# Kernel tuning notes

Measured on AMD Instinct MI355X. Metric: run time of the kernel, lower is better.

## Reference

```python
import math
import jax, jax.numpy as jnp
import numpy as np

B, L, NS = 8, 1024, 512
D, NH, DN = 512, 8, 256
E, K, HE = 8, 2, 2048
EPS = 1e-5


def setup_inputs() -> dict:
    key = jax.random.key(0)
    ks = jax.random.split(key, 40)
    def rn(i, shape, s=0.02):
        return jax.random.normal(ks[i], shape, jnp.float32) * s
    inp = {
        'x': jax.random.normal(ks[0], (B, L, D), jnp.float32),
        'scene_tokens': jax.random.normal(ks[1], (B, NS, D), jnp.float32),
        't': jax.random.uniform(ks[2], (B,), jnp.float32) * 1000.0,
        # scene LayerNorm (affine)
        'scene_norm_g': jnp.ones((D,), jnp.float32),
        'scene_norm_b': jnp.zeros((D,), jnp.float32),
        # scene cross-attn projections (stored [in,out])
        'ca_wq': rn(3, (D, D)), 'ca_bq': jnp.zeros((D,)),
        'ca_wk': rn(4, (D, D)), 'ca_bk': jnp.zeros((D,)),
        'ca_wv': rn(5, (D, D)), 'ca_bv': jnp.zeros((D,)),
        'ca_wo': rn(6, (D, D)), 'ca_bo': jnp.zeros((D,)),
        # self-attn projections
        'sa_wq': rn(7, (D, D)), 'sa_bq': jnp.zeros((D,)),
        'sa_wk': rn(8, (D, D)), 'sa_bk': jnp.zeros((D,)),
        'sa_wv': rn(9, (D, D)), 'sa_bv': jnp.zeros((D,)),
        'sa_wo': rn(10, (D, D)), 'sa_bo': jnp.zeros((D,)),
        # noise_embed MLP: Linear(D,DN) -> SiLU -> Linear(DN,DN)
        'ne_w1': rn(11, (D, DN)), 'ne_b1': jnp.zeros((DN,)),
        'ne_w2': rn(12, (DN, DN)), 'ne_b2': jnp.zeros((DN,)),
        # AdaLN modulations: Linear(DN, 2D)
        'ncsa_mod_w': rn(13, (DN, 2 * D)), 'ncsa_mod_b': jnp.zeros((2 * D,)),
        'moe_mod_w': rn(14, (DN, 2 * D)), 'moe_mod_b': jnp.zeros((2 * D,)),
        # router
        'router_w': rn(15, (DN, E), s=0.1),
        # stacked pose-branch experts: fc_in D->2*HE, fc_out HE->D
        'fc_in_w': rn(16, (E, D, 2 * HE)), 'fc_in_b': jnp.zeros((E, 2 * HE)),
        'fc_out_w': rn(17, (E, HE, D)), 'fc_out_b': jnp.zeros((E, D)),
    }
    return inp


def _ln(x):
    mu = x.mean(-1, keepdims=True)
    var = ((x - mu) ** 2).mean(-1, keepdims=True)
    return (x - mu) * jax.lax.rsqrt(var + EPS)


def _mha(q_in, k_in, v_in, wq, bq, wk, bk, wv, bv, wo, bo):
    b, lq, d = q_in.shape
    lk = k_in.shape[1]
    hd = d // NH
    q = (q_in @ wq + bq).reshape(b, lq, NH, hd)
    k = (k_in @ wk + bk).reshape(b, lk, NH, hd)
    v = (v_in @ wv + bv).reshape(b, lk, NH, hd)
    att = jnp.einsum('bqhd,bkhd->bhqk', q, k) / math.sqrt(hd)
    p = jax.nn.softmax(att, axis=-1)
    o = jnp.einsum('bhqk,bkhd->bqhd', p, v).reshape(b, lq, d)
    return o @ wo + bo


def reference(x, scene_tokens, t,
              scene_norm_g, scene_norm_b,
              ca_wq, ca_bq, ca_wk, ca_bk, ca_wv, ca_bv, ca_wo, ca_bo,
              sa_wq, sa_bq, sa_wk, sa_bk, sa_wv, sa_bv, sa_wo, sa_bo,
              ne_w1, ne_b1, ne_w2, ne_b2,
              ncsa_mod_w, ncsa_mod_b, moe_mod_w, moe_mod_b,
              router_w, fc_in_w, fc_in_b, fc_out_w, fc_out_b):
    # --- noise clock embedding: sinusoidal(t, D) -> MLP ---
    half = D // 2
    freqs = jnp.exp(-math.log(10000.0) * jnp.arange(half, dtype=jnp.float32) / (half - 1))
    ang = t[:, None] * freqs[None, :]
    temb = jnp.concatenate([jnp.cos(ang), jnp.sin(ang)], axis=-1)  # [B, D]
    nc = jax.nn.silu(temb @ ne_w1 + ne_b1) @ ne_w2 + ne_b2  # [B, DN]

    # --- scene cross-attention ---
    x_in = _ln(x) * scene_norm_g + scene_norm_b
    x = x + _mha(x_in, scene_tokens, scene_tokens,
                 ca_wq, ca_bq, ca_wk, ca_bk, ca_wv, ca_bv, ca_wo, ca_bo)

    # --- noise-conditioned self-attention (AdaLN) ---
    mod = nc @ ncsa_mod_w + ncsa_mod_b
    shift, scale = jnp.split(mod, 2, axis=-1)
    x_ncsa = _ln(x) * (1.0 + scale[:, None, :]) + shift[:, None, :]
    x = x + _mha(x_ncsa, x_ncsa, x_ncsa,
                 sa_wq, sa_bq, sa_wk, sa_bk, sa_wv, sa_bv, sa_wo, sa_bo)

    # --- pose branch: AdaLN + noise-conditioned MoE ---
    mod = nc @ moe_mod_w + moe_mod_b
    shift, scale = jnp.split(mod, 2, axis=-1)
    x_moe = _ln(x) * (1.0 + scale[:, None, :]) + shift[:, None, :]

    logits = nc @ router_w  # temperature = 1.0
    probs = jax.nn.softmax(logits, axis=-1)
    tw, ti = jax.lax.top_k(probs, K)  # [B,K]
    tw = tw / jnp.clip(tw.sum(-1, keepdims=True), 1e-8)

    # gather per-sample selected expert weights -> grouped GEMM
    Wi = fc_in_w[ti]   # [B,K,D,2HE]
    bi = fc_in_b[ti]   # [B,K,2HE]
    h = jnp.einsum('bld,bkdh->bklh', x_moe, Wi) + bi[:, :, None, :]
    val, gate = jnp.split(h, 2, axis=-1)
    hid = val * jax.nn.silu(gate)   # [B,K,L,HE]
    Wo = fc_out_w[ti]  # [B,K,HE,D]
    bo = fc_out_b[ti]  # [B,K,D]
    eo = jnp.einsum('bklh,bkhd->bkld', hid, Wo) + bo[:, :, None, :]
    mixed = jnp.einsum('bk,bkld->bld', tw, eo)

    return x + mixed
```

## Files before the change

kernel.cpp:

```cpp
#include <hip/hip_runtime.h>
#include <math.h>

typedef unsigned short ushort_t;
typedef __attribute__((ext_vector_type(8))) short short8;
typedef __attribute__((ext_vector_type(4))) float f32x4;

#define B_   8
#define L_   1024
#define NS_  512
#define D_   512
#define NH_  8
#define HE_  2048
#define EPS_ 1e-5f

#define MFMA16(a, b, c) __builtin_amdgcn_mfma_f32_16x16x32_bf16(a, b, c, 0, 0, 0)
#define GL2LDS(g, l) __builtin_amdgcn_global_load_lds( \
    (const __attribute__((address_space(1))) unsigned int*)(g), \
    (__attribute__((address_space(3))) unsigned int*)(l), 16, 0, 0)

__device__ __forceinline__ ushort_t f2bf(float f) {
  unsigned u = __float_as_uint(f);
  unsigned r = (u + 0x7fffu + ((u >> 16) & 1u)) >> 16;
  return (ushort_t)r;
}

__device__ __forceinline__ void stage_tile(const ushort_t* __restrict__ g0,
                                           int ld, ushort_t* lds) {
  const int t = threadIdx.x;
  const int w = t >> 6, lane = t & 63;
#pragma unroll
  for (int j = 0; j < 2; ++j) {
    const int c = w * 64 + j * 256 + lane;
    const int row = c >> 2, col = (c & 3) * 8;
    GL2LDS(g0 + (size_t)row * ld + col, lds + (size_t)(w * 64 + j * 256) * 8);
  }
}

__global__ __launch_bounds__(256) void noise_embed(
    const float* __restrict__ t_in,
    const float* __restrict__ w1, const float* __restrict__ b1,
    const float* __restrict__ w2, const float* __restrict__ b2,
    const float* __restrict__ rw,
    float* __restrict__ nc_out,
    float* __restrict__ tw_out, int* __restrict__ ti_out)
{
  const int b = blockIdx.x;
  const int t = threadIdx.x;
  __shared__ float temb[512];
  __shared__ float h1[256];
  __shared__ float ncs[256];
  const float tv = t_in[b];
  {
    float fr = __expf(-logf(10000.0f) * (float)t / 255.0f);
    float ang = tv * fr;
    temb[t] = cosf(ang);
    temb[256 + t] = sinf(ang);
  }
  __syncthreads();
  {
    float s = b1[t];
#pragma unroll 8
    for (int i = 0; i < 512; ++i) s += temb[i] * w1[i * 256 + t];
    h1[t] = s / (1.0f + __expf(-s));
  }
  __syncthreads();
  {
    float s = b2[t];
#pragma unroll 8
    for (int i = 0; i < 256; ++i) s += h1[i] * w2[i * 256 + t];
    ncs[t] = s;
    nc_out[b * 256 + t] = s;
  }
  __syncthreads();
  if (t == 0) {
    float lg[8];
    for (int e = 0; e < 8; ++e) {
      float s = 0.f;
      for (int i = 0; i < 256; ++i) s += ncs[i] * rw[i * 8 + e];
      lg[e] = s;
    }
    float mx = lg[0];
    for (int e = 1; e < 8; ++e) mx = fmaxf(mx, lg[e]);
    float z = 0.f, p[8];
    for (int e = 0; e < 8; ++e) { p[e] = __expf(lg[e] - mx); z += p[e]; }
    for (int e = 0; e < 8; ++e) p[e] /= z;
    int i0 = 0;
    for (int e = 1; e < 8; ++e) if (p[e] > p[i0]) i0 = e;
    int i1 = (i0 == 0) ? 1 : 0;
    for (int e = 0; e < 8; ++e) if (e != i0 && p[e] > p[i1]) i1 = e;
    float s01 = fmaxf(p[i0] + p[i1], 1e-8f);
    tw_out[b * 2 + 0] = p[i0] / s01;
    tw_out[b * 2 + 1] = p[i1] / s01;
    ti_out[b * 2 + 0] = i0;
    ti_out[b * 2 + 1] = i1;
  }
}

__global__ __launch_bounds__(256) void mod_proj(
    const float* __restrict__ nc,
    const float* __restrict__ ncsa_w, const float* __restrict__ ncsa_b,
    const float* __restrict__ moe_w, const float* __restrict__ moe_b,
    float* __restrict__ ncsa_mod, float* __restrict__ moe_mod)
{
  const int b = blockIdx.x, cg = blockIdx.y;
  const int t = threadIdx.x;
  __shared__ float ncs[256];
  ncs[t] = nc[b * 256 + t];
  __syncthreads();
  const int col = cg * 128 + (t & 127);
  const int half = t >> 7;
  const float* wsel = half ? moe_w : ncsa_w;
  const float* bsel = half ? moe_b : ncsa_b;
  float* osel = half ? moe_mod : ncsa_mod;
  float s = bsel[col];
#pragma unroll 8
  for (int i = 0; i < 256; ++i) s += ncs[i] * wsel[(size_t)i * 1024 + col];
  osel[b * 1024 + col] = s;
}

__global__ __launch_bounds__(256) void ln_mod_kernel(
    const float* __restrict__ X, const float* __restrict__ gvec,
    const float* __restrict__ bvec, const float* __restrict__ mod,
    ushort_t* __restrict__ Y)
{
  const int row = blockIdx.x;
  const int b = row >> 10;
  const int t = threadIdx.x;
  const float* xr = X + (size_t)row * 512;
  float2 v = *(const float2*)(xr + t * 2);
  float s = v.x + v.y;
  float q = v.x * v.x + v.y * v.y;
#pragma unroll
  for (int off = 32; off > 0; off >>= 1) {
    s += __shfl_down(s, off, 64);
    q += __shfl_down(q, off, 64);
  }
  __shared__ float ws_[4], wq_[4], smu[1], sinv[1];
  if ((t & 63) == 0) { ws_[t >> 6] = s; wq_[t >> 6] = q; }
  __syncthreads();
  if (t == 0) {
    float S = ws_[0] + ws_[1] + ws_[2] + ws_[3];
    float Q = wq_[0] + wq_[1] + wq_[2] + wq_[3];
    float mu = S * (1.0f / 512.0f);
    float var = Q * (1.0f / 512.0f) - mu * mu;
    smu[0] = mu;
    sinv[0] = rsqrtf(var + EPS_);
  }
  __syncthreads();
  const float mu = smu[0], inv = sinv[0];
  const int d0 = t * 2;
  float scx, scy, shx, shy;
  if (mod) {
    const float* mrow = mod + (size_t)b * 1024;
    scx = 1.0f + mrow[512 + d0]; scy = 1.0f + mrow[512 + d0 + 1];
    shx = mrow[d0];              shy = mrow[d0 + 1];
  } else {
    scx = gvec[d0]; scy = gvec[d0 + 1];
    shx = bvec[d0]; shy = bvec[d0 + 1];
  }
  float ox = (v.x - mu) * inv * scx + shx;
  float oy = (v.y - mu) * inv * scy + shy;
  unsigned pk = (unsigned)f2bf(ox) | ((unsigned)f2bf(oy) << 16);
  *(unsigned*)(Y + (size_t)row * 512 + d0) = pk;
}

__global__ __launch_bounds__(256) void transpose_cvt(
    const float* __restrict__ in, ushort_t* __restrict__ out,
    int R, int C, long ibs, long obs)
{
  __shared__ float tile[32][33];
  const float* src = in + (size_t)blockIdx.z * ibs;
  ushort_t* dst = out + (size_t)blockIdx.z * obs;
  const int c0 = blockIdx.x * 32, r0 = blockIdx.y * 32;
  const int tx = threadIdx.x & 31, ty = threadIdx.x >> 5;
  for (int rr = ty; rr < 32; rr += 8)
    tile[rr][tx] = src[(size_t)(r0 + rr) * C + c0 + tx];
  __syncthreads();
  for (int rr = ty; rr < 32; rr += 8)
    dst[(size_t)(c0 + rr) * R + r0 + tx] = f2bf(tile[tx][rr]);
}

struct P8 { const float* p[8]; };
__global__ __launch_bounds__(256) void transpose_cvt8(
    P8 srcs, ushort_t* __restrict__ out)
{
  __shared__ float tile[32][33];
  const float* src = srcs.p[blockIdx.z];
  ushort_t* dst = out + (size_t)blockIdx.z * 512 * 512;
  const int c0 = blockIdx.x * 32, r0 = blockIdx.y * 32;
  const int tx = threadIdx.x & 31, ty = threadIdx.x >> 5;
  for (int rr = ty; rr < 32; rr += 8)
    tile[rr][tx] = src[(size_t)(r0 + rr) * 512 + c0 + tx];
  __syncthreads();
  for (int rr = ty; rr < 32; rr += 8)
    dst[(size_t)(c0 + rr) * 512 + r0 + tx] = f2bf(tile[tx][rr]);
}

__global__ __launch_bounds__(256) void cvt_bf16(
    const float* __restrict__ in, ushort_t* __restrict__ out)
{
  const int i = (blockIdx.x * 256 + threadIdx.x) * 4;
  float4 v = *(const float4*)(in + i);
  uint2 pk;
  pk.x = (unsigned)f2bf(v.x) | ((unsigned)f2bf(v.y) << 16);
  pk.y = (unsigned)f2bf(v.z) | ((unsigned)f2bf(v.w) << 16);
  *(uint2*)(out + i) = pk;
}

__global__ __launch_bounds__(256) void gemm_bf16(
    const ushort_t* __restrict__ A, const ushort_t* __restrict__ Bt,
    const float* __restrict__ bias, const float* __restrict__ resid,
    void* __restrict__ Cout, int M, int N, int K, int bf16_out)
{
  __shared__ ushort_t As[2][4096];
  __shared__ ushort_t Bs[2][4096];
  const int t = threadIdx.x;
  const int w = t >> 6, lane = t & 63;
  const int quad = lane >> 4, r = lane & 15;
  const int wm = w >> 1, wn = w & 1;
  const int bm = blockIdx.y * 128, bn = blockIdx.x * 128;
  f32x4 acc[4][4];
#pragma unroll
  for (int i = 0; i < 4; ++i)
#pragma unroll
    for (int j = 0; j < 4; ++j) acc[i][j] = (f32x4){0.f, 0.f, 0.f, 0.f};
  const ushort_t* Ab = A + (size_t)bm * K;
  const ushort_t* Bb = Bt + (size_t)bn * K;
  const int NIT = K >> 5;
  stage_tile(Ab, K, As[0]);
  stage_tile(Bb, K, Bs[0]);
  __syncthreads();
  for (int it = 0; it < NIT; ++it) {
    const int cur = it & 1;
    if (it + 1 < NIT) {
      stage_tile(Ab + (it + 1) * 32, K, As[cur ^ 1]);
      stage_tile(Bb + (it + 1) * 32, K, Bs[cur ^ 1]);
    }
    short8 af[4], bfg[4];
#pragma unroll
    for (int i = 0; i < 4; ++i)
      af[i] = *(const short8*)&As[cur][(wm * 64 + i * 16 + r) * 32 + quad * 8];
#pragma unroll
    for (int j = 0; j < 4; ++j)
      bfg[j] = *(const short8*)&Bs[cur][(wn * 64 + j * 16 + r) * 32 + quad * 8];
#pragma unroll
    for (int i = 0; i < 4; ++i)
#pragma unroll
      for (int j = 0; j < 4; ++j)
        acc[i][j] = MFMA16(af[i], bfg[j], acc[i][j]);
    __syncthreads();
  }
  if (bf16_out) {
    ushort_t* Cb = (ushort_t*)Cout;
#pragma unroll
    for (int j = 0; j < 4; ++j) {
      const int col = bn + wn * 64 + j * 16 + r;
      const float bia = bias[col];
#pragma unroll
      for (int i = 0; i < 4; ++i)
#pragma unroll
        for (int reg = 0; reg < 4; ++reg) {
          const int row = bm + wm * 64 + i * 16 + quad * 4 + reg;
          Cb[(size_t)row * N + col] = f2bf(acc[i][j][reg] + bia);
        }
    }
  } else {
    float* Cf = (float*)Cout;
#pragma unroll
    for (int j = 0; j < 4; ++j) {
      const int col = bn + wn * 64 + j * 16 + r;
      const float bia = bias[col];
#pragma unroll
      for (int i = 0; i < 4; ++i)
#pragma unroll
        for (int reg = 0; reg < 4; ++reg) {
          const int row = bm + wm * 64 + i * 16 + quad * 4 + reg;
          float v = acc[i][j][reg] + bia;
          if (resid) v += resid[(size_t)row * N + col];
          Cf[(size_t)row * N + col] = v;
        }
    }
  }
}

__global__ __launch_bounds__(256, 2) void fattn_mfma(
    const ushort_t* __restrict__ Q, const ushort_t* __restrict__ Kmat,
    const ushort_t* __restrict__ V, ushort_t* __restrict__ O, int Lk)
{
  __shared__ __align__(16) ushort_t Ks[64][72];
  __shared__ __align__(16) ushort_t Vt[64][72];
  __shared__ __align__(16) ushort_t Pt[4][32][72];
  const int t = threadIdx.x;
  const int w = t >> 6, lane = t & 63;
  const int quad = lane >> 4, r = lane & 15;
  const int h = blockIdx.y, b = blockIdx.z;
  const int q0 = blockIdx.x * 128;
  const size_t hoff = (size_t)h * 64;
  const ushort_t* Qb = Q + ((size_t)b * 1024 + q0) * 512 + hoff;
  const ushort_t* Kb = Kmat + (size_t)b * Lk * 512 + hoff;
  const ushort_t* Vb = V + (size_t)b * Lk * 512 + hoff;

  short8 qb[2][2];
#pragma unroll
  for (int ct = 0; ct < 2; ++ct)
#pragma unroll
    for (int ki = 0; ki < 2; ++ki)
      qb[ct][ki] = *(const short8*)(Qb + (size_t)(w * 32 + ct * 16 + r) * 512 +
                                    ki * 32 + quad * 8);

  f32x4 oacc[4][2];
#pragma unroll
  for (int rt = 0; rt < 4; ++rt)
#pragma unroll
    for (int ct = 0; ct < 2; ++ct) oacc[rt][ct] = (f32x4){0.f, 0.f, 0.f, 0.f};
  float m_[2] = {-1e30f, -1e30f};
  float l_[2] = {0.f, 0.f};

  uint4 kr[2], vr[2], kn[2], vn[2];
  auto ldkv = [&](int k0, uint4* kp, uint4* vp) {
#pragma unroll
    for (int j = 0; j < 2; ++j) {
      const int dof = (w + 4 * j) * 8;
      kp[j] = *(const uint4*)(Kb + (size_t)(k0 + lane) * 512 + dof);
      vp[j] = *(const uint4*)(Vb + (size_t)(k0 + lane) * 512 + dof);
    }
  };
  auto stkv = [&](const uint4* kp, const uint4* vp) {
#pragma unroll
    for (int j = 0; j < 2; ++j) {
      const int dof = (w + 4 * j) * 8;
      *(uint4*)&Ks[lane][dof] = kp[j];
      const ushort_t* vv = (const ushort_t*)&vp[j];
#pragma unroll
      for (int i = 0; i < 8; ++i) Vt[dof + i][lane] = vv[i];
    }
  };

  ldkv(0, kr, vr);
  const int nch = Lk >> 6;
  for (int c = 0; c < nch; ++c) {
    stkv(kr, vr);
    __syncthreads();
    if (c + 1 < nch) ldkv((c + 1) << 6, kn, vn);

    f32x4 sacc[4][2];
#pragma unroll
    for (int rt = 0; rt < 4; ++rt)
#pragma unroll
      for (int ct = 0; ct < 2; ++ct) sacc[rt][ct] = (f32x4){0.f, 0.f, 0.f, 0.f};
#pragma unroll
    for (int ki = 0; ki < 2; ++ki) {
      short8 kf[4];
#pragma unroll
      for (int rt = 0; rt < 4; ++rt)
        kf[rt] = *(const short8*)&Ks[rt * 16 + r][ki * 32 + quad * 8];
#pragma unroll
      for (int rt = 0; rt < 4; ++rt)
#pragma unroll
        for (int ct = 0; ct < 2; ++ct)
          sacc[rt][ct] = MFMA16(kf[rt], qb[ct][ki], sacc[rt][ct]);
    }

#pragma unroll
    for (int ct = 0; ct < 2; ++ct) {
      float vmax = sacc[0][ct][0];
#pragma unroll
      for (int rt = 0; rt < 4; ++rt)
#pragma unroll
        for (int reg = 0; reg < 4; ++reg) vmax = fmaxf(vmax, sacc[rt][ct][reg]);
      vmax = fmaxf(vmax, __shfl_xor(vmax, 16, 64));
      vmax = fmaxf(vmax, __shfl_xor(vmax, 32, 64));
      const float mnew = fmaxf(m_[ct], vmax * 0.125f);
      const float corr = __expf(m_[ct] - mnew);
      m_[ct] = mnew;
      float ps = 0.f;
#pragma unroll
      for (int rt = 0; rt < 4; ++rt) {
        float p0 = __expf(fmaf(sacc[rt][ct][0], 0.125f, -mnew));
        float p1 = __expf(fmaf(sacc[rt][ct][1], 0.125f, -mnew));
        float p2 = __expf(fmaf(sacc[rt][ct][2], 0.125f, -mnew));
        float p3 = __expf(fmaf(sacc[rt][ct][3], 0.125f, -mnew));
        ps += (p0 + p1) + (p2 + p3);
        uint2 pk;
        pk.x = (unsigned)f2bf(p0) | ((unsigned)f2bf(p1) << 16);
        pk.y = (unsigned)f2bf(p2) | ((unsigned)f2bf(p3) << 16);
        *(uint2*)&Pt[w][ct * 16 + r][rt * 16 + quad * 4] = pk;
      }
      ps += __shfl_xor(ps, 16, 64);
      ps += __shfl_xor(ps, 32, 64);
      l_[ct] = l_[ct] * corr + ps;
#pragma unroll
      for (int rt = 0; rt < 4; ++rt)
#pragma unroll
        for (int reg = 0; reg < 4; ++reg) oacc[rt][ct][reg] *= corr;
    }

#pragma unroll
    for (int ki = 0; ki < 2; ++ki) {
      short8 vf[4], pf[2];
#pragma unroll
      for (int rt = 0; rt < 4; ++rt)
        vf[rt] = *(const short8*)&Vt[rt * 16 + r][ki * 32 + quad * 8];
#pragma unroll
      for (int ct = 0; ct < 2; ++ct)
        pf[ct] = *(const short8*)&Pt[w][ct * 16 + r][ki * 32 + quad * 8];
#pragma unroll
      for (int rt = 0; rt < 4; ++rt)
#pragma unroll
        for (int ct = 0; ct < 2; ++ct)
          oacc[rt][ct] = MFMA16(vf[rt], pf[ct], oacc[rt][ct]);
    }
    __syncthreads();
#pragma unroll
    for (int j = 0; j < 2; ++j) { kr[j] = kn[j]; vr[j] = vn[j]; }
  }

#pragma unroll
  for (int ct = 0; ct < 2; ++ct) {
    const float inv = 1.0f / l_[ct];
    const int qg = q0 + w * 32 + ct * 16 + r;
    ushort_t* op = O + ((size_t)b * 1024 + qg) * 512 + hoff;
#pragma unroll
    for (int rt = 0; rt < 4; ++rt) {
      uint2 pk;
      pk.x = (unsigned)f2bf(oacc[rt][ct][0] * inv) |
             ((unsigned)f2bf(oacc[rt][ct][1] * inv) << 16);
      pk.y = (unsigned)f2bf(oacc[rt][ct][2] * inv) |
             ((unsigned)f2bf(oacc[rt][ct][3] * inv) << 16);
      *(uint2*)(op + rt * 16 + quad * 4) = pk;
    }
  }
}

__global__ __launch_bounds__(256) void moe_fcin(
    const ushort_t* __restrict__ Xm, const ushort_t* __restrict__ WiT,
    const float* __restrict__ Bi, const float* __restrict__ tw,
    const int* __restrict__ ti, ushort_t* __restrict__ Hid, int ks)
{
  __shared__ ushort_t As[2][4096];
  __shared__ ushort_t Bv[2][4096];
  __shared__ ushort_t Bg[2][4096];
  const int t = threadIdx.x;
  const int w = t >> 6, lane = t & 63;
  const int quad = lane >> 4, r = lane & 15;
  const int wm = w >> 1, wn = w & 1;
  const int b = blockIdx.z;
  const int e = ti[b * 2 + ks];
  const float wq = tw[b * 2 + ks];
  const int r0 = blockIdx.y * 128, n0 = blockIdx.x * 128;
  const ushort_t* Ab = Xm + ((size_t)b * 1024 + r0) * 512;
  const ushort_t* Wv = WiT + (size_t)e * 4096 * 512 + (size_t)n0 * 512;
  const ushort_t* Wg = Wv + (size_t)2048 * 512;
  f32x4 av[4][4], ag[4][4];
#pragma unroll
  for (int i = 0; i < 4; ++i)
#pragma unroll
    for (int j = 0; j < 4; ++j) {
      av[i][j] = (f32x4){0.f, 0.f, 0.f, 0.f};
      ag[i][j] = (f32x4){0.f, 0.f, 0.f, 0.f};
    }
  stage_tile(Ab, 512, As[0]);
  stage_tile(Wv, 512, Bv[0]);
  stage_tile(Wg, 512, Bg[0]);
  __syncthreads();
  for (int it = 0; it < 16; ++it) {
    const int cur = it & 1;
    if (it + 1 < 16) {
      stage_tile(Ab + (it + 1) * 32, 512, As[cur ^ 1]);
      stage_tile(Wv + (it + 1) * 32, 512, Bv[cur ^ 1]);
      stage_tile(Wg + (it + 1) * 32, 512, Bg[cur ^ 1]);
    }
    short8 af[4], bv[4], bg[4];
#pragma unroll
    for (int i = 0; i < 4; ++i)
      af[i] = *(const short8*)&As[cur][(wm * 64 + i * 16 + r) * 32 + quad * 8];
#pragma unroll
    for (int j = 0; j < 4; ++j) {
      bv[j] = *(const short8*)&Bv[cur][(wn * 64 + j * 16 + r) * 32 + quad * 8];
      bg[j] = *(const short8*)&Bg[cur][(wn * 64 + j * 16 + r) * 32 + quad * 8];
    }
#pragma unroll
    for (int i = 0; i < 4; ++i)
#pragma unroll
      for (int j = 0; j < 4; ++j) {
        av[i][j] = MFMA16(af[i], bv[j], av[i][j]);
        ag[i][j] = MFMA16(af[i], bg[j], ag[i][j]);
      }
    __syncthreads();
  }
  ushort_t* Hb = Hid + (size_t)b * 1024 * 2048;
#pragma unroll
  for (int j = 0; j < 4; ++j) {
    const int col = n0 + wn * 64 + j * 16 + r;
    const float bval = Bi[(size_t)e * 4096 + col];
    const float bgat = Bi[(size_t)e * 4096 + 2048 + col];
#pragma unroll
    for (int i = 0; i < 4; ++i)
#pragma unroll
      for (int reg = 0; reg < 4; ++reg) {
        const int lrow = r0 + wm * 64 + i * 16 + quad * 4 + reg;
        float vv = av[i][j][reg] + bval;
        float gg = ag[i][j][reg] + bgat;
        float hv = vv * (gg / (1.0f + __expf(-gg))) * wq;
        Hb[(size_t)lrow * 2048 + col] = f2bf(hv);
      }
  }
}

__global__ __launch_bounds__(256) void moe_fcout(
    const ushort_t* __restrict__ Hid, const ushort_t* __restrict__ WoT,
    const float* __restrict__ Bo, const float* __restrict__ X2,
    const float* __restrict__ tw, const int* __restrict__ ti,
    float* __restrict__ Out, int ks, int first)
{
  __shared__ ushort_t As[2][4096];
  __shared__ ushort_t Bs[2][4096];
  const int t = threadIdx.x;
  const int w = t >> 6, lane = t & 63;
  const int quad = lane >> 4, r = lane & 15;
  const int wm = w >> 1, wn = w & 1;
  const int b = blockIdx.z;
  const int e = ti[b * 2 + ks];
  const int r0 = blockIdx.y * 128, n0 = blockIdx.x * 128;
  f32x4 acc[4][4];
#pragma unroll
  for (int i = 0; i < 4; ++i)
#pragma unroll
    for (int j = 0; j < 4; ++j) acc[i][j] = (f32x4){0.f, 0.f, 0.f, 0.f};
  const ushort_t* Ab = Hid + ((size_t)b * 1024 + r0) * 2048;
  const ushort_t* Bb = WoT + (size_t)e * 512 * 2048 + (size_t)n0 * 2048;
  stage_tile(Ab, 2048, As[0]);
  stage_tile(Bb, 2048, Bs[0]);
  __syncthreads();
  for (int it = 0; it < 64; ++it) {
    const int cur = it & 1;
    if (it + 1 < 64) {
      stage_tile(Ab + (it + 1) * 32, 2048, As[cur ^ 1]);
      stage_tile(Bb + (it + 1) * 32, 2048, Bs[cur ^ 1]);
    }
    short8 af[4], bfg[4];
#pragma unroll
    for (int i = 0; i < 4; ++i)
      af[i] = *(const short8*)&As[cur][(wm * 64 + i * 16 + r) * 32 + quad * 8];
#pragma unroll
    for (int j = 0; j < 4; ++j)
      bfg[j] = *(const short8*)&Bs[cur][(wn * 64 + j * 16 + r) * 32 + quad * 8];
#pragma unroll
    for (int i = 0; i < 4; ++i)
#pragma unroll
      for (int j = 0; j < 4; ++j)
        acc[i][j] = MFMA16(af[i], bfg[j], acc[i][j]);
    __syncthreads();
  }
  const int e0 = ti[b * 2], e1 = ti[b * 2 + 1];
  const float tw0 = tw[b * 2], tw1 = tw[b * 2 + 1];
#pragma unroll
  for (int j = 0; j < 4; ++j) {
    const int col = n0 + wn * 64 + j * 16 + r;
    const float badd = first ? (tw0 * Bo[(size_t)e0 * 512 + col] +
                                tw1 * Bo[(size_t)e1 * 512 + col]) : 0.f;
#pragma unroll
    for (int i = 0; i < 4; ++i)
#pragma unroll
      for (int reg = 0; reg < 4; ++reg) {
        const size_t row = (size_t)b * 1024 + r0 + wm * 64 + i * 16 + quad * 4 + reg;
        const size_t idx = row * 512 + col;
        const float base = first ? X2[idx] : Out[idx];
        Out[idx] = base + acc[i][j][reg] + badd;
      }
  }
}

extern "C" void kernel_launch(void* const* d_in, const int* in_sizes, int n_in,
                              void* d_out, int out_size, void* d_ws, size_t ws_size,
                              hipStream_t stream) {
  const float* x        = (const float*)d_in[0];
  const float* scene    = (const float*)d_in[1];
  const float* t_in     = (const float*)d_in[2];
  const float* sn_g     = (const float*)d_in[3];
  const float* sn_b     = (const float*)d_in[4];
  const float* ca_wq    = (const float*)d_in[5];
  const float* ca_bq    = (const float*)d_in[6];
  const float* ca_wk    = (const float*)d_in[7];
  const float* ca_bk    = (const float*)d_in[8];
  const float* ca_wv    = (const float*)d_in[9];
  const float* ca_bv    = (const float*)d_in[10];
  const float* ca_wo    = (const float*)d_in[11];
  const float* ca_bo    = (const float*)d_in[12];
  const float* sa_wq    = (const float*)d_in[13];
  const float* sa_bq    = (const float*)d_in[14];
  const float* sa_wk    = (const float*)d_in[15];
  const float* sa_bk    = (const float*)d_in[16];
  const float* sa_wv    = (const float*)d_in[17];
  const float* sa_bv    = (const float*)d_in[18];
  const float* sa_wo    = (const float*)d_in[19];
  const float* sa_bo    = (const float*)d_in[20];
  const float* ne_w1    = (const float*)d_in[21];
  const float* ne_b1    = (const float*)d_in[22];
  const float* ne_w2    = (const float*)d_in[23];
  const float* ne_b2    = (const float*)d_in[24];
  const float* ncsa_w   = (const float*)d_in[25];
  const float* ncsa_b   = (const float*)d_in[26];
  const float* moe_w    = (const float*)d_in[27];
  const float* moe_b    = (const float*)d_in[28];
  const float* router_w = (const float*)d_in[29];
  const float* fc_in_w  = (const float*)d_in[30];
  const float* fc_in_b  = (const float*)d_in[31];
  const float* fc_out_w = (const float*)d_in[32];
  const float* fc_out_b = (const float*)d_in[33];
  float* out = (float*)d_out;

  char* W = (char*)d_ws;
  const size_t MB = 1u << 20;
  float* ncsa_mod = (float*)W;
  float* moe_mod  = ncsa_mod + 8192;
  float* tw       = moe_mod + 8192;
  int*   ti       = (int*)(tw + 16);
  float* nc_ws    = (float*)(ti + 16);
  ushort_t* wT      = (ushort_t*)(W + 1 * MB);
  ushort_t* fciT    = (ushort_t*)(W + 5 * MB);
  ushort_t* fcoT    = (ushort_t*)(W + 37 * MB);
  ushort_t* xin_bf  = (ushort_t*)(W + 53 * MB);
  ushort_t* attn_bf = xin_bf;
  ushort_t* scene_bf= (ushort_t*)(W + 61 * MB);
  ushort_t* qf = (ushort_t*)(W + 65 * MB);
  ushort_t* kf = (ushort_t*)(W + 73 * MB);
  ushort_t* vf = (ushort_t*)(W + 81 * MB);
  ushort_t* hid = (ushort_t*)(W + 61 * MB);
  float* x1 = out;

  const int WSZ = 512 * 512;

  noise_embed<<<dim3(B_), dim3(256), 0, stream>>>(
      t_in, ne_w1, ne_b1, ne_w2, ne_b2, router_w, nc_ws, tw, ti);
  mod_proj<<<dim3(B_, 8), dim3(256), 0, stream>>>(
      nc_ws, ncsa_w, ncsa_b, moe_w, moe_b, ncsa_mod, moe_mod);

  P8 dsrc;
  dsrc.p[0] = ca_wq; dsrc.p[1] = ca_wk; dsrc.p[2] = ca_wv; dsrc.p[3] = ca_wo;
  dsrc.p[4] = sa_wq; dsrc.p[5] = sa_wk; dsrc.p[6] = sa_wv; dsrc.p[7] = sa_wo;
  transpose_cvt8<<<dim3(16, 16, 8), 256, 0, stream>>>(dsrc, wT);
  transpose_cvt<<<dim3(128, 16, 8), 256, 0, stream>>>(fc_in_w, fciT, 512, 4096,
                                                      (long)512 * 4096, (long)512 * 4096);
  transpose_cvt<<<dim3(16, 64, 8), 256, 0, stream>>>(fc_out_w, fcoT, 2048, 512,
                                                     (long)2048 * 512, (long)2048 * 512);
  cvt_bf16<<<dim3(2048), 256, 0, stream>>>(scene, scene_bf);

  ln_mod_kernel<<<dim3(8192), 256, 0, stream>>>(x, sn_g, sn_b, nullptr, xin_bf);
  gemm_bf16<<<dim3(4, 64), 256, 0, stream>>>(xin_bf, wT + 0 * WSZ, ca_bq, nullptr, qf, 8192, 512, 512, 1);
  gemm_bf16<<<dim3(4, 32), 256, 0, stream>>>(scene_bf, wT + 1 * WSZ, ca_bk, nullptr, kf, 4096, 512, 512, 1);
  gemm_bf16<<<dim3(4, 32), 256, 0, stream>>>(scene_bf, wT + 2 * WSZ, ca_bv, nullptr, vf, 4096, 512, 512, 1);
  fattn_mfma<<<dim3(8, NH_, B_), 256, 0, stream>>>(qf, kf, vf, attn_bf, NS_);
  gemm_bf16<<<dim3(4, 64), 256, 0, stream>>>(attn_bf, wT + 3 * WSZ, ca_bo, x, x1, 8192, 512, 512, 0);

  ln_mod_kernel<<<dim3(8192), 256, 0, stream>>>(x1, nullptr, nullptr, ncsa_mod, xin_bf);
  gemm_bf16<<<dim3(4, 64), 256, 0, stream>>>(xin_bf, wT + 4 * WSZ, sa_bq, nullptr, qf, 8192, 512, 512, 1);
  gemm_bf16<<<dim3(4, 64), 256, 0, stream>>>(xin_bf, wT + 5 * WSZ, sa_bk, nullptr, kf, 8192, 512, 512, 1);
  gemm_bf16<<<dim3(4, 64), 256, 0, stream>>>(xin_bf, wT + 6 * WSZ, sa_bv, nullptr, vf, 8192, 512, 512, 1);
  fattn_mfma<<<dim3(8, NH_, B_), 256, 0, stream>>>(qf, kf, vf, attn_bf, L_);
  gemm_bf16<<<dim3(4, 64), 256, 0, stream>>>(attn_bf, wT + 7 * WSZ, sa_bo, out, out, 8192, 512, 512, 0);

  ln_mod_kernel<<<dim3(8192), 256, 0, stream>>>(out, nullptr, nullptr, moe_mod, xin_bf);
  moe_fcin<<<dim3(16, 8, B_), 256, 0, stream>>>(xin_bf, fciT, fc_in_b, tw, ti, hid, 0);
  moe_fcout<<<dim3(4, 8, B_), 256, 0, stream>>>(hid, fcoT, fc_out_b, out, tw, ti, out, 0, 1);
  moe_fcin<<<dim3(16, 8, B_), 256, 0, stream>>>(xin_bf, fciT, fc_in_b, tw, ti, hid, 1);
  moe_fcout<<<dim3(4, 8, B_), 256, 0, stream>>>(hid, fcoT, fc_out_b, out, tw, ti, out, 1, 0);
}
```

Before: 832.8 us.

## Fuse QKV projections, remap attention blocks by XCD, lazy softmax rescale

Merges the separate Q/K/V (and cross-attn K/V) projection GEMMs into single wider GEMMs by relying on the transposed weights being contiguous, with a per-512-column bias pointer table, and gives the attention kernel strided Q/K/V access. The attention grid becomes 1D with an XCD-aware mapping so blocks for the same batch/head share cache, adds s_setprio around MFMA phases, and skips the online-softmax rescale unless the running max grows by more than a threshold. noise_embed and mod_proj use 1024 threads with split-K reductions over shuffles. This cuts launch count and per-kernel overhead, at the cost of more complex indexing and a threshold-based rescale that changes numerics slightly.

```diff
diff --git a/kernel.cpp b/kernel.cpp
--- a/kernel.cpp
+++ b/kernel.cpp
@@ -36,7 +36,7 @@
   }
 }
 
-__global__ __launch_bounds__(256) void noise_embed(
+__global__ __launch_bounds__(1024) void noise_embed(
     const float* __restrict__ t_in,
     const float* __restrict__ w1, const float* __restrict__ b1,
     const float* __restrict__ w2, const float* __restrict__ b2,
@@ -49,36 +49,57 @@
   __shared__ float temb[512];
   __shared__ float h1[256];
   __shared__ float ncs[256];
+  __shared__ float lg[8];
   const float tv = t_in[b];
+  if (t < 512) {
+    const int k = t & 255;
+    float fr = __expf(-logf(10000.0f) * (float)k / 255.0f);
+    float ang = tv * fr;
+    temb[t] = (t < 256) ? cosf(ang) : sinf(ang);
+  }
+  __syncthreads();
+  const int col = t >> 2, part = t & 3;
   {
-    float fr = __expf(-logf(10000.0f) * (float)t / 255.0f);
-    float ang = tv * fr;
-    temb[t] = cosf(ang);
-    temb[256 + t] = sinf(ang);
+    float s = 0.f;
+    const float* wp = w1 + (size_t)(part * 128) * 256 + col;
+    const float* tp = temb + part * 128;
+#pragma unroll 32
+    for (int i = 0; i < 128; ++i) s += tp[i] * wp[(size_t)i * 256];
+    s += __shfl_xor(s, 1, 64);
+    s += __shfl_xor(s, 2, 64);
+    if (part == 0) {
+      s += b1[col];
+      h1[col] = s / (1.0f + __expf(-s));
+    }
   }
   __syncthreads();
   {
-    float s = b1[t];
-#pragma unroll 8
-    for (int i = 0; i < 512; ++i) s += temb[i] * w1[i * 256 + t];
-    h1[t] = s / (1.0f + __expf(-s));
-  }
-  __syncthreads();
-  {
-    float s = b2[t];
-#pragma unroll 8
-    for (int i = 0; i < 256; ++i) s += h1[i] * w2[i * 256 + t];
-    ncs[t] = s;
-    nc_out[b * 256 + t] = s;
+    float s = 0.f;
+    const float* wp = w2 + (size_t)(part * 64) * 256 + col;
+    const float* hp = h1 + part * 64;
+#pragma unroll 32
+    for (int i = 0; i < 64; ++i) s += hp[i] * wp[(size_t)i * 256];
+    s += __shfl_xor(s, 1, 64);
+    s += __shfl_xor(s, 2, 64);
+    if (part == 0) {
+      s += b2[col];
+      ncs[col] = s;
+      nc_out[b * 256 + col] = s;
+    }
+  }
+  __syncthreads();
+  if (t < 64) {
+    const int e = t >> 3, seg = t & 7;
+    float s = 0.f;
+#pragma unroll
+    for (int i = 0; i < 32; ++i) s += ncs[seg * 32 + i] * rw[(seg * 32 + i) * 8 + e];
+    s += __shfl_xor(s, 1, 64);
+    s += __shfl_xor(s, 2, 64);
+    s += __shfl_xor(s, 4, 64);
+    if (seg == 0) lg[e] = s;
   }
   __syncthreads();
   if (t == 0) {
-    float lg[8];
-    for (int e = 0; e < 8; ++e) {
-      float s = 0.f;
-      for (int i = 0; i < 256; ++i) s += ncs[i] * rw[i * 8 + e];
-      lg[e] = s;
-    }
     float mx = lg[0];
     for (int e = 1; e < 8; ++e) mx = fmaxf(mx, lg[e]);
     float z = 0.f, p[8];
@@ -96,7 +117,7 @@
   }
 }
 
-__global__ __launch_bounds__(256) void mod_proj(
+__global__ __launch_bounds__(1024) void mod_proj(
     const float* __restrict__ nc,
     const float* __restrict__ ncsa_w, const float* __restrict__ ncsa_b,
     const float* __restrict__ moe_w, const float* __restrict__ moe_b,
@@ -105,17 +126,24 @@
   const int b = blockIdx.x, cg = blockIdx.y;
   const int t = threadIdx.x;
   __shared__ float ncs[256];
-  ncs[t] = nc[b * 256 + t];
-  __syncthreads();
-  const int col = cg * 128 + (t & 127);
-  const int half = t >> 7;
+  if (t < 256) ncs[t] = nc[b * 256 + t];
+  __syncthreads();
+  const int idx = t >> 2, part = t & 3;
+  const int half = idx >> 7;
+  const int col = cg * 128 + (idx & 127);
   const float* wsel = half ? moe_w : ncsa_w;
-  const float* bsel = half ? moe_b : ncsa_b;
-  float* osel = half ? moe_mod : ncsa_mod;
-  float s = bsel[col];
-#pragma unroll 8
-  for (int i = 0; i < 256; ++i) s += ncs[i] * wsel[(size_t)i * 1024 + col];
-  osel[b * 1024 + col] = s;
+  float s = 0.f;
+  const float* wp = wsel + (size_t)(part * 64) * 1024 + col;
+  const float* np = ncs + part * 64;
+#pragma unroll 32
+  for (int i = 0; i < 64; ++i) s += np[i] * wp[(size_t)i * 1024];
+  s += __shfl_xor(s, 1, 64);
+  s += __shfl_xor(s, 2, 64);
+  if (part == 0) {
+    const float* bsel = half ? moe_b : ncsa_b;
+    float* osel = half ? moe_mod : ncsa_mod;
+    osel[b * 1024 + col] = s + bsel[col];
+  }
 }
 
 __global__ __launch_bounds__(256) void ln_mod_kernel(
@@ -207,9 +235,10 @@
   *(uint2*)(out + i) = pk;
 }
 
+struct B3 { const float* p[3]; };
 __global__ __launch_bounds__(256) void gemm_bf16(
     const ushort_t* __restrict__ A, const ushort_t* __restrict__ Bt,
-    const float* __restrict__ bias, const float* __restrict__ resid,
+    B3 bias, const float* __restrict__ resid,
     void* __restrict__ Cout, int M, int N, int K, int bf16_out)
 {
   __shared__ ushort_t As[2][4096];
@@ -255,7 +284,7 @@
 #pragma unroll
     for (int j = 0; j < 4; ++j) {
       const int col = bn + wn * 64 + j * 16 + r;
-      const float bia = bias[col];
+      const float bia = bias.p[col >> 9][col & 511];
 #pragma unroll
       for (int i = 0; i < 4; ++i)
 #pragma unroll
@@ -269,7 +298,7 @@
 #pragma unroll
     for (int j = 0; j < 4; ++j) {
       const int col = bn + wn * 64 + j * 16 + r;
-      const float bia = bias[col];
+      const float bia = bias.p[col >> 9][col & 511];
 #pragma unroll
       for (int i = 0; i < 4; ++i)
 #pragma unroll
@@ -285,7 +314,8 @@
 
 __global__ __launch_bounds__(256, 2) void fattn_mfma(
     const ushort_t* __restrict__ Q, const ushort_t* __restrict__ Kmat,
-    const ushort_t* __restrict__ V, ushort_t* __restrict__ O, int Lk)
+    const ushort_t* __restrict__ V, ushort_t* __restrict__ O, int Lk,
+    int ldq, int ldkv)
 {
   __shared__ __align__(16) ushort_t Ks[64][72];
   __shared__ __align__(16) ushort_t Vt[64][72];
@@ -293,19 +323,23 @@
   const int t = threadIdx.x;
   const int w = t >> 6, lane = t & 63;
   const int quad = lane >> 4, r = lane & 15;
-  const int h = blockIdx.y, b = blockIdx.z;
-  const int q0 = blockIdx.x * 128;
+  const int bid = blockIdx.x;
+  const int xcd = bid & 7, jj = bid >> 3;
+  const int qi = jj & 7;
+  const int g = xcd + 8 * (jj >> 3);
+  const int h = g & 7, b = g >> 3;
+  const int q0 = qi * 128;
   const size_t hoff = (size_t)h * 64;
-  const ushort_t* Qb = Q + ((size_t)b * 1024 + q0) * 512 + hoff;
-  const ushort_t* Kb = Kmat + (size_t)b * Lk * 512 + hoff;
-  const ushort_t* Vb = V + (size_t)b * Lk * 512 + hoff;
+  const ushort_t* Qb = Q + ((size_t)b * 1024 + q0) * ldq + hoff;
+  const ushort_t* Kb = Kmat + (size_t)b * Lk * ldkv + hoff;
+  const ushort_t* Vb = V + (size_t)b * Lk * ldkv + hoff;
 
   short8 qb[2][2];
 #pragma unroll
   for (int ct = 0; ct < 2; ++ct)
 #pragma unroll
     for (int ki = 0; ki < 2; ++ki)
-      qb[ct][ki] = *(const short8*)(Qb + (size_t)(w * 32 + ct * 16 + r) * 512 +
+      qb[ct][ki] = *(const short8*)(Qb + (size_t)(w * 32 + ct * 16 + r) * ldq +
                                     ki * 32 + quad * 8);
 
   f32x4 oacc[4][2];
@@ -317,12 +351,12 @@
   float l_[2] = {0.f, 0.f};
 
   uint4 kr[2], vr[2], kn[2], vn[2];
-  auto ldkv = [&](int k0, uint4* kp, uint4* vp) {
+  auto ldkvf = [&](int k0, uint4* kp, uint4* vp) {
 #pragma unroll
     for (int j = 0; j < 2; ++j) {
       const int dof = (w + 4 * j) * 8;
-      kp[j] = *(const uint4*)(Kb + (size_t)(k0 + lane) * 512 + dof);
-      vp[j] = *(const uint4*)(Vb + (size_t)(k0 + lane) * 512 + dof);
+      kp[j] = *(const uint4*)(Kb + (size_t)(k0 + lane) * ldkv + dof);
+      vp[j] = *(const uint4*)(Vb + (size_t)(k0 + lane) * ldkv + dof);
     }
   };
   auto stkv = [&](const uint4* kp, const uint4* vp) {
@@ -336,18 +370,19 @@
     }
   };
 
-  ldkv(0, kr, vr);
+  ldkvf(0, kr, vr);
   const int nch = Lk >> 6;
   for (int c = 0; c < nch; ++c) {
     stkv(kr, vr);
     __syncthreads();
-    if (c + 1 < nch) ldkv((c + 1) << 6, kn, vn);
+    if (c + 1 < nch) ldkvf((c + 1) << 6, kn, vn);
 
     f32x4 sacc[4][2];
 #pragma unroll
     for (int rt = 0; rt < 4; ++rt)
 #pragma unroll
       for (int ct = 0; ct < 2; ++ct) sacc[rt][ct] = (f32x4){0.f, 0.f, 0.f, 0.f};
+    __builtin_amdgcn_s_setprio(1);
 #pragma unroll
     for (int ki = 0; ki < 2; ++ki) {
       short8 kf[4];
@@ -360,7 +395,9 @@
         for (int ct = 0; ct < 2; ++ct)
           sacc[rt][ct] = MFMA16(kf[rt], qb[ct][ki], sacc[rt][ct]);
     }
-
+    __builtin_amdgcn_s_setprio(0);
+
+    float pm[2];
 #pragma unroll
     for (int ct = 0; ct < 2; ++ct) {
       float vmax = sacc[0][ct][0];
@@ -370,16 +407,32 @@
         for (int reg = 0; reg < 4; ++reg) vmax = fmaxf(vmax, sacc[rt][ct][reg]);
       vmax = fmaxf(vmax, __shfl_xor(vmax, 16, 64));
       vmax = fmaxf(vmax, __shfl_xor(vmax, 32, 64));
-      const float mnew = fmaxf(m_[ct], vmax * 0.125f);
-      const float corr = __expf(m_[ct] - mnew);
-      m_[ct] = mnew;
+      pm[ct] = vmax * 0.125f;
+    }
+    const bool need = (pm[0] > m_[0] + 8.f) || (pm[1] > m_[1] + 8.f);
+    if (__any(need)) {
+#pragma unroll
+      for (int ct = 0; ct < 2; ++ct) {
+        const float mnew = fmaxf(m_[ct], pm[ct]);
+        const float corr = __expf(m_[ct] - mnew);
+        m_[ct] = mnew;
+        l_[ct] *= corr;
+#pragma unroll
+        for (int rt = 0; rt < 4; ++rt)
+#pragma unroll
+          for (int reg = 0; reg < 4; ++reg) oacc[rt][ct][reg] *= corr;
+      }
+    }
+#pragma unroll
+    for (int ct = 0; ct < 2; ++ct) {
+      const float mcur = m_[ct];
       float ps = 0.f;
 #pragma unroll
       for (int rt = 0; rt < 4; ++rt) {
-        float p0 = __expf(fmaf(sacc[rt][ct][0], 0.125f, -mnew));
-        float p1 = __expf(fmaf(sacc[rt][ct][1], 0.125f, -mnew));
-        float p2 = __expf(fmaf(sacc[rt][ct][2], 0.125f, -mnew));
-        float p3 = __expf(fmaf(sacc[rt][ct][3], 0.125f, -mnew));
+        float p0 = __expf(fmaf(sacc[rt][ct][0], 0.125f, -mcur));
+        float p1 = __expf(fmaf(sacc[rt][ct][1], 0.125f, -mcur));
+        float p2 = __expf(fmaf(sacc[rt][ct][2], 0.125f, -mcur));
+        float p3 = __expf(fmaf(sacc[rt][ct][3], 0.125f, -mcur));
         ps += (p0 + p1) + (p2 + p3);
         uint2 pk;
         pk.x = (unsigned)f2bf(p0) | ((unsigned)f2bf(p1) << 16);
@@ -388,13 +441,10 @@
       }
       ps += __shfl_xor(ps, 16, 64);
       ps += __shfl_xor(ps, 32, 64);
-      l_[ct] = l_[ct] * corr + ps;
-#pragma unroll
-      for (int rt = 0; rt < 4; ++rt)
-#pragma unroll
-        for (int reg = 0; reg < 4; ++reg) oacc[rt][ct][reg] *= corr;
-    }
-
+      l_[ct] += ps;
+    }
+
+    __builtin_amdgcn_s_setprio(1);
 #pragma unroll
     for (int ki = 0; ki < 2; ++ki) {
       short8 vf[4], pf[2];
@@ -410,6 +460,7 @@
         for (int ct = 0; ct < 2; ++ct)
           oacc[rt][ct] = MFMA16(vf[rt], pf[ct], oacc[rt][ct]);
     }
+    __builtin_amdgcn_s_setprio(0);
     __syncthreads();
 #pragma unroll
     for (int j = 0; j < 2; ++j) { kr[j] = kn[j]; vr[j] = vn[j]; }
@@ -623,17 +674,17 @@
   ushort_t* xin_bf  = (ushort_t*)(W + 53 * MB);
   ushort_t* attn_bf = xin_bf;
   ushort_t* scene_bf= (ushort_t*)(W + 61 * MB);
-  ushort_t* qf = (ushort_t*)(W + 65 * MB);
-  ushort_t* kf = (ushort_t*)(W + 73 * MB);
-  ushort_t* vf = (ushort_t*)(W + 81 * MB);
+  ushort_t* cq  = (ushort_t*)(W + 65 * MB);
+  ushort_t* ckv = (ushort_t*)(W + 73 * MB);
+  ushort_t* qkv = (ushort_t*)(W + 65 * MB);
   ushort_t* hid = (ushort_t*)(W + 61 * MB);
   float* x1 = out;
 
   const int WSZ = 512 * 512;
 
-  noise_embed<<<dim3(B_), dim3(256), 0, stream>>>(
+  noise_embed<<<dim3(B_), dim3(1024), 0, stream>>>(
       t_in, ne_w1, ne_b1, ne_w2, ne_b2, router_w, nc_ws, tw, ti);
-  mod_proj<<<dim3(B_, 8), dim3(256), 0, stream>>>(
+  mod_proj<<<dim3(B_, 8), dim3(1024), 0, stream>>>(
       nc_ws, ncsa_w, ncsa_b, moe_w, moe_b, ncsa_mod, moe_mod);
 
   P8 dsrc;
@@ -646,19 +697,21 @@
                                                      (long)2048 * 512, (long)2048 * 512);
   cvt_bf16<<<dim3(2048), 256, 0, stream>>>(scene, scene_bf);
 
+  B3 bq1 = {{ca_bq, ca_bq, ca_bq}};
+  B3 bkv = {{ca_bk, ca_bv, ca_bv}};
+  B3 bo3 = {{ca_bo, ca_bo, ca_bo}};
   ln_mod_kernel<<<dim3(8192), 256, 0, stream>>>(x, sn_g, sn_b, nullptr, xin_bf);
-  gemm_bf16<<<dim3(4, 64), 256, 0, stream>>>(xin_bf, wT + 0 * WSZ, ca_bq, nullptr, qf, 8192, 512, 512, 1);
-  gemm_bf16<<<dim3(4, 32), 256, 0, stream>>>(scene_bf, wT + 1 * WSZ, ca_bk, nullptr, kf, 4096, 512, 512, 1);
-  gemm_bf16<<<dim3(4, 32), 256, 0, stream>>>(scene_bf, wT + 2 * WSZ, ca_bv, nullptr, vf, 4096, 512, 512, 1);
-  fattn_mfma<<<dim3(8, NH_, B_), 256, 0, stream>>>(qf, kf, vf, attn_bf, NS_);
-  gemm_bf16<<<dim3(4, 64), 256, 0, stream>>>(attn_bf, wT + 3 * WSZ, ca_bo, x, x1, 8192, 512, 512, 0);
-
+  gemm_bf16<<<dim3(4, 64), 256, 0, stream>>>(xin_bf, wT + 0 * WSZ, bq1, nullptr, cq, 8192, 512, 512, 1);
+  gemm_bf16<<<dim3(8, 32), 256, 0, stream>>>(scene_bf, wT + 1 * WSZ, bkv, nullptr, ckv, 4096, 1024, 512, 1);
+  fattn_mfma<<<dim3(512), 256, 0, stream>>>(cq, ckv, ckv + 512, attn_bf, NS_, 512, 1024);
+  gemm_bf16<<<dim3(4, 64), 256, 0, stream>>>(attn_bf, wT + 3 * WSZ, bo3, x, x1, 8192, 512, 512, 0);
+
+  B3 bqkv = {{sa_bq, sa_bk, sa_bv}};
+  B3 bso = {{sa_bo, sa_bo, sa_bo}};
   ln_mod_kernel<<<dim3(8192), 256, 0, stream>>>(x1, nullptr, nullptr, ncsa_mod, xin_bf);
-  gemm_bf16<<<dim3(4, 64), 256, 0, stream>>>(xin_bf, wT + 4 * WSZ, sa_bq, nullptr, qf, 8192, 512, 512, 1);
-  gemm_bf16<<<dim3(4, 64), 256, 0, stream>>>(xin_bf, wT + 5 * WSZ, sa_bk, nullptr, kf, 8192, 512, 512, 1);
-  gemm_bf16<<<dim3(4, 64), 256, 0, stream>>>(xin_bf, wT + 6 * WSZ, sa_bv, nullptr, vf, 8192, 512, 512, 1);
-  fattn_mfma<<<dim3(8, NH_, B_), 256, 0, stream>>>(qf, kf, vf, attn_bf, L_);
-  gemm_bf16<<<dim3(4, 64), 256, 0, stream>>>(attn_bf, wT + 7 * WSZ, sa_bo, out, out, 8192, 512, 512, 0);
+  gemm_bf16<<<dim3(12, 64), 256, 0, stream>>>(xin_bf, wT + 4 * WSZ, bqkv, nullptr, qkv, 8192, 1536, 512, 1);
+  fattn_mfma<<<dim3(512), 256, 0, stream>>>(qkv, qkv + 512, qkv + 1024, attn_bf, L_, 1536, 1536);
+  gemm_bf16<<<dim3(4, 64), 256, 0, stream>>>(attn_bf, wT + 7 * WSZ, bso, out, out, 8192, 512, 512, 0);
 
   ln_mod_kernel<<<dim3(8192), 256, 0, stream>>>(out, nullptr, nullptr, moe_mod, xin_bf);
   moe_fcin<<<dim3(16, 8, B_), 256, 0, stream>>>(xin_bf, fciT, fc_in_b, tw, ti, hid, 0);
```

Measured after the change: 754.7 us. -9.4%, faster.
